# Optimization experiments

Measured on AMD Instinct MI355X. Metric: run time of the kernel, lower is better.

Reference implementation:

```python
import jax, jax.numpy as jnp
import numpy as np

MIN_NORM = 1e-15
BALL_EPS = 1e-5  # keep points strictly inside the unit ball (c = 1)


def _artanh(x):
    return jnp.arctanh(jnp.clip(x, -1.0 + BALL_EPS, 1.0 - BALL_EPS))


def expmap0(u):
    # Poincare ball exp map at the origin, c = 1
    n = jnp.clip(jnp.linalg.norm(u, axis=-1, keepdims=True), MIN_NORM)
    return jnp.tanh(n) * u / n


def mobius_matvec(M, x):
    # Mobius matrix-vector product applied to every row of x: [N, D] -> [N, D]
    x_n = jnp.clip(jnp.linalg.norm(x, axis=-1, keepdims=True), MIN_NORM)
    Mx = x @ M.T
    Mx_n = jnp.clip(jnp.linalg.norm(Mx, axis=-1, keepdims=True), MIN_NORM)
    return jnp.tanh(Mx_n / x_n * _artanh(x_n)) * Mx / Mx_n


def pairwise_sqdist(x):
    # sqdist(x_i, x_j) for all pairs via mobius_add(-x_i, x_j); x: [N, D] -> [N, N]
    u = -x[:, None, :]          # [N, 1, D]
    v = x[None, :, :]           # [1, N, D]
    xy = jnp.sum(u * v, axis=-1, keepdims=True)   # [N, N, 1]
    x2 = jnp.sum(u * u, axis=-1, keepdims=True)
    y2 = jnp.sum(v * v, axis=-1, keepdims=True)
    num = (1.0 + 2.0 * xy + y2) * u + (1.0 - x2) * v   # [N, N, D]
    den = jnp.clip(1.0 + 2.0 * xy + x2 * y2, MIN_NORM)
    ma_n = jnp.linalg.norm(num / den, axis=-1)          # [N, N]
    d = 2.0 * _artanh(ma_n)
    return d * d


def setup_inputs() -> dict:
    key = jax.random.key(0)
    k1, k2, k3 = jax.random.split(key, 3)
    N, D, L = 512, 256, 2
    H_euc = jax.random.normal(k1, (N, D), dtype=jnp.float32)
    att_W = jax.random.normal(k2, (L, D, D), dtype=jnp.float32) / np.sqrt(D)
    A = jax.random.randint(k3, (N, N), 0, 2).astype(bool)
    return {"H_euc": H_euc, "att_W": att_W, "A": A}


def reference(H_euc, att_W, A):
    H = expmap0(H_euc)                      # [N, D] on the Poincare ball
    L = att_W.shape[0]
    for l in range(L):
        Wh = mobius_matvec(att_W[l], H)     # one mobius matvec per node (hoisted out of the i,j loop)
        scores = pairwise_sqdist(Wh)        # [N, N] hyperbolic squared distances
        scores = jnp.where(A, scores, -10000.0)
        att = jax.nn.softmax(scores, axis=1)
        att = jnp.where(A, att, 0.0)
        H = att @ H                         # [N, D]
    return H
```

## Files before the change

kernel.cpp:

```cpp
#include <hip/hip_runtime.h>
#include <math.h>

#define NN 512
#define DD 256

#define FMA4(P, S, V) \
  P.x = fmaf(S, (V).x, P.x); P.y = fmaf(S, (V).y, P.y); \
  P.z = fmaf(S, (V).z, P.z); P.w = fmaf(S, (V).w, P.w);

__device__ __forceinline__ void wred_sum2(double& a, double& b){
  #pragma unroll
  for (int o = 32; o > 0; o >>= 1){
    a += __shfl_down(a, o);
    b += __shfl_down(b, o);
  }
}
__device__ void bred_sum2(double& a, double& b){
  __shared__ double sa[4], sb[4]; __shared__ double ra, rb;
  int lane = threadIdx.x & 63, w = threadIdx.x >> 6;
  wred_sum2(a, b);
  __syncthreads();
  if (lane == 0){ sa[w] = a; sb[w] = b; }
  __syncthreads();
  if (threadIdx.x == 0){
    ra = (sa[0] + sa[1]) + (sa[2] + sa[3]);
    rb = (sb[0] + sb[1]) + (sb[2] + sb[3]);
  }
  __syncthreads();
  a = ra; b = rb;
}

__device__ __forceinline__ double artanh_clip(double x){
  const double lim = 1.0 - 1e-5;
  if (x >  lim) x =  lim;
  if (x < -lim) x = -lim;
  return 0.5 * log((1.0 + x) / (1.0 - x));
}

__global__ __launch_bounds__(256) void transpose_k(const float* __restrict__ W,
                                                   float* __restrict__ W0T,
                                                   float* __restrict__ W1T){
  __shared__ float tile[64][65];
  int b = blockIdx.x, t = threadIdx.x;
  const float* src = (b < 16) ? W : (W + DD * DD);
  float* dst = (b < 16) ? W0T : W1T;
  int tb = b & 15, tr = tb >> 2, tc = tb & 3;
  int tx = t & 63, ty4 = t >> 6;
  #pragma unroll
  for (int yy = 0; yy < 64; yy += 4)
    tile[yy + ty4][tx] = src[(tr * 64 + yy + ty4) * DD + tc * 64 + tx];
  __syncthreads();
  #pragma unroll
  for (int yy = 0; yy < 64; yy += 4)
    dst[(tc * 64 + yy + ty4) * DD + tr * 64 + tx] = tile[tx][yy + ty4];
}

__global__ __launch_bounds__(256) void matvec0_k(
    const float* __restrict__ Hin, const float* __restrict__ W0T,
    float* __restrict__ Hf, float* __restrict__ Wh, float* __restrict__ WhT,
    double* __restrict__ r2){
  int b = blockIdx.x, t = threadIdx.x;
  int i0 = 2 * b, i1 = i0 + 1;
  __shared__ float h0s[DD], h1s[DD];
  __shared__ float4 mp[512];
  float u0 = Hin[i0 * DD + t], u1 = Hin[i1 * DD + t];
  double n0 = (double)u0 * (double)u0, n1 = (double)u1 * (double)u1;
  bred_sum2(n0, n1);
  n0 = sqrt(n0); if (n0 < 1e-15) n0 = 1e-15;
  n1 = sqrt(n1); if (n1 < 1e-15) n1 = 1e-15;
  double t0 = tanh(n0), t1 = tanh(n1);
  float h0 = (float)(t0 / n0 * (double)u0);
  float h1 = (float)(t1 / n1 * (double)u1);
  Hf[i0 * DD + t] = h0; Hf[i1 * DD + t] = h1;
  double xn0 = t0 < 1e-15 ? 1e-15 : t0;
  double xn1 = t1 < 1e-15 ? 1e-15 : t1;
  h0s[t] = h0; h1s[t] = h1;
  __syncthreads();
  {
    int ks = t >> 6, dq = t & 63;
    const float4* WT4 = (const float4*)W0T;
    float4 p0 = {0,0,0,0}, p1 = {0,0,0,0};
    int k0 = ks * 64;
    #pragma unroll 8
    for (int kk = 0; kk < 64; kk++){
      int k = k0 + kk;
      float4 wv = WT4[k * 64 + dq];
      float a0 = h0s[k], a1 = h1s[k];
      FMA4(p0, a0, wv)
      FMA4(p1, a1, wv)
    }
    mp[(ks * 64 + dq) * 2 + 0] = p0;
    mp[(ks * 64 + dq) * 2 + 1] = p1;
  }
  __syncthreads();
  const float* pf = (const float*)mp;
  int base = (t >> 2) * 8 + (t & 3);
  float mx0 = (pf[base]     + pf[base +  512]) + (pf[base + 1024] + pf[base + 1536]);
  float mx1 = (pf[base + 4] + pf[base +  516]) + (pf[base + 1028] + pf[base + 1540]);
  double m0 = (double)mx0 * (double)mx0, m1 = (double)mx1 * (double)mx1;
  bred_sum2(m0, m1);
  double mn0 = sqrt(m0); if (mn0 < 1e-15) mn0 = 1e-15;
  double mn1 = sqrt(m1); if (mn1 < 1e-15) mn1 = 1e-15;
  double th0 = tanh(mn0 / xn0 * artanh_clip(xn0));
  double th1 = tanh(mn1 / xn1 * artanh_clip(xn1));
  float w0 = (float)((double)mx0 * (th0 / mn0));
  float w1 = (float)((double)mx1 * (th1 / mn1));
  Wh[i0 * DD + t] = w0;  Wh[i1 * DD + t] = w1;
  WhT[t * NN + i0] = w0; WhT[t * NN + i1] = w1;
  if (t == 0){ r2[i0] = th0 * th0; r2[i1] = th1 * th1; }
}

template<bool LAST>
__global__ __launch_bounds__(512) void fused_k(
    const float* __restrict__ Wh, const float* __restrict__ WhT,
    const double* __restrict__ r2, const int* __restrict__ A,
    const float* __restrict__ H, const float* __restrict__ WT2,
    float* __restrict__ Hn, float* __restrict__ Whn,
    float* __restrict__ WhTn, double* __restrict__ r2n){
  int b = blockIdx.x, tid = threadIdx.x;
  int i0 = 2 * b;
  __shared__ float xs[2 * DD];
  __shared__ float a_s[2][NN];
  __shared__ float4 parts[1024];
  __shared__ double ssum[8];
  __shared__ float hn_s[2][DD];
  __shared__ double hnorm2[2];

  xs[tid] = Wh[i0 * DD + tid];
  __syncthreads();

  {
    int ks = tid >> 7, jq = tid & 127;
    const float4* WT4 = (const float4*)WhT;
    const float4* x04 = (const float4*)xs;
    const float4* x14 = (const float4*)(xs + DD);
    float4 p0 = {0,0,0,0}, p1 = {0,0,0,0};
    int kq0 = ks * 16;
    #pragma unroll 4
    for (int kk = 0; kk < 16; kk++){
      float4 xa = x04[kq0 + kk], xb = x14[kq0 + kk];
      const float4* wp = WT4 + (kq0 + kk) * 4 * 128 + jq;
      float4 wa = wp[0], wb = wp[128], wc = wp[256], wd = wp[384];
      FMA4(p0, xa.x, wa) FMA4(p0, xa.y, wb) FMA4(p0, xa.z, wc) FMA4(p0, xa.w, wd)
      FMA4(p1, xb.x, wa) FMA4(p1, xb.y, wb) FMA4(p1, xb.z, wc) FMA4(p1, xb.w, wd)
    }
    parts[(ks * 128 + jq) * 2 + 0] = p0;
    parts[(ks * 128 + jq) * 2 + 1] = p1;
  }
  __syncthreads();

  int sgC = tid >> 6, qC = tid & 63;
  const float4* H4 = (const float4*)H;
  float4 hpre[8];
  #pragma unroll
  for (int jj = 0; jj < 8; jj++) hpre[jj] = H4[(sgC * 64 + jj) * 64 + qC];

  int r = tid >> 8, j2 = tid & 255;
  int i = i0 + r;
  double X2 = r2[i];
  const float* pf = (const float*)parts;
  auto dsum = [&](int j) -> double {
    int base = (((j >> 2) * 2 + r) << 2) + (j & 3);
    return ((double)pf[base] + (double)pf[base + 1024])
         + ((double)pf[base + 2048] + (double)pf[base + 3072]);
  };
  double d0 = dsum(j2), d1 = dsum(j2 + 256);

  auto score = [&](double dot, double Y2, int jj) -> double {
    if (i == jj) return 0.0;
    double xy = -dot;
    double a  = 1.0 + 2.0 * xy + Y2;
    double bb = 1.0 - X2;
    double den = 1.0 + 2.0 * xy + X2 * Y2;
    if (den < 1e-15) den = 1e-15;
    double nn = a * a * X2 + 2.0 * a * bb * xy + bb * bb * Y2;
    if (nn < 0.0) nn = 0.0;
    double s = sqrt(nn);
    double smax = den * (1.0 - 1e-5);
    if (s > smax) s = smax;
    double d = log((den + s) / (den - s));
    return d * d;
  };

  double Y0 = r2[j2], Y1 = r2[j2 + 256];
  int m0 = A[i * NN + j2], m1 = A[i * NN + j2 + 256];
  double e0 = 0.0, e1 = 0.0;
  if (m0) e0 = exp(score(d0, Y0, j2) - 150.0);
  if (m1) e1 = exp(score(d1, Y1, j2 + 256) - 150.0);

  double part = e0 + e1;
  #pragma unroll
  for (int o = 32; o > 0; o >>= 1) part += __shfl_down(part, o);
  int w = tid >> 6, lane = tid & 63;
  if (lane == 0) ssum[w] = part;
  __syncthreads();
  int base4 = r * 4;
  double sum = (ssum[base4] + ssum[base4 + 1]) + (ssum[base4 + 2] + ssum[base4 + 3]);
  double inv = 1.0 / sum;
  a_s[r][j2]       = m0 ? (float)(e0 * inv) : 0.f;
  a_s[r][j2 + 256] = m1 ? (float)(e1 * inv) : 0.f;
  __syncthreads();

  {
    float4 c0 = {0,0,0,0}, c1 = {0,0,0,0};
    int jb = sgC * 64;
    #pragma unroll
    for (int jj = 0; jj < 8; jj++){
      int j = jb + jj;
      float a0 = a_s[0][j], a1 = a_s[1][j];
      float4 h = hpre[jj];
      FMA4(c0, a0, h) FMA4(c1, a1, h)
    }
    #pragma unroll 8
    for (int jj = 8; jj < 64; jj++){
      int j = jb + jj;
      float a0 = a_s[0][j], a1 = a_s[1][j];
      float4 h = H4[j * 64 + qC];
      FMA4(c0, a0, h) FMA4(c1, a1, h)
    }
    parts[sgC * 64 + qC]       = c0;
    parts[512 + sgC * 64 + qC] = c1;
  }
  __syncthreads();
  if (tid < 128){
    int rr = tid >> 6, qq = tid & 63;
    float4 p[8];
    #pragma unroll
    for (int s8 = 0; s8 < 8; s8++) p[s8] = parts[rr * 512 + s8 * 64 + qq];
    float4 o;
    o.x = ((p[0].x + p[1].x) + (p[2].x + p[3].x)) + ((p[4].x + p[5].x) + (p[6].x + p[7].x));
    o.y = ((p[0].y + p[1].y) + (p[2].y + p[3].y)) + ((p[4].y + p[5].y) + (p[6].y + p[7].y));
    o.z = ((p[0].z + p[1].z) + (p[2].z + p[3].z)) + ((p[4].z + p[5].z) + (p[6].z + p[7].z));
    o.w = ((p[0].w + p[1].w) + (p[2].w + p[3].w)) + ((p[4].w + p[5].w) + (p[6].w + p[7].w));
    ((float4*)(Hn + (i0 + rr) * DD))[qq] = o;
    if (!LAST){
      ((float4*)hn_s[rr])[qq] = o;
      double s = (double)o.x * o.x + (double)o.y * o.y
               + (double)o.z * o.z + (double)o.w * o.w;
      #pragma unroll
      for (int off = 32; off > 0; off >>= 1) s += __shfl_down(s, off);
      if (qq == 0) hnorm2[rr] = s;
    }
  }
  if (LAST) return;
  __syncthreads();

  {
    int ks2 = tid >> 6, dq = tid & 63;
    const float4* WT4b = (const float4*)WT2;
    const float* h0 = hn_s[0]; const float* h1 = hn_s[1];
    float4 p0 = {0,0,0,0}, p1 = {0,0,0,0};
    int k0 = ks2 * 32;
    #pragma unroll 8
    for (int kk = 0; kk < 32; kk++){
      int k = k0 + kk;
      float4 wv = WT4b[k * 64 + dq];
      float a0v = h0[k], a1v = h1[k];
      FMA4(p0, a0v, wv) FMA4(p1, a1v, wv)
    }
    parts[(ks2 * 64 + dq) * 2 + 0] = p0;
    parts[(ks2 * 64 + dq) * 2 + 1] = p1;
  }
  __syncthreads();
  {
    int rr = tid >> 8, d = tid & 255;
    const float* pf2 = (const float*)parts;
    int base = ((d >> 2) * 2 + rr) * 4 + (d & 3);
    float q0 = pf2[base]        + pf2[base + 512];
    float q1 = pf2[base + 1024] + pf2[base + 1536];
    float q2 = pf2[base + 2048] + pf2[base + 2560];
    float q3 = pf2[base + 3072] + pf2[base + 3584];
    float mx = (q0 + q1) + (q2 + q3);
    double m2 = (double)mx * (double)mx;
    #pragma unroll
    for (int o = 32; o > 0; o >>= 1) m2 += __shfl_down(m2, o);
    int w2 = tid >> 6, lane2 = tid & 63;
    if (lane2 == 0) ssum[w2] = m2;
    __syncthreads();
    int b4 = rr * 4;
    double m2sum = (ssum[b4] + ssum[b4 + 1]) + (ssum[b4 + 2] + ssum[b4 + 3]);
    double mn = sqrt(m2sum); if (mn < 1e-15) mn = 1e-15;
    double xn = sqrt(hnorm2[rr]); if (xn < 1e-15) xn = 1e-15;
    double th = tanh(mn / xn * artanh_clip(xn));
    float wv = (float)((double)mx * (th / mn));
    int irow = i0 + rr;
    Whn[irow * DD + d] = wv;
    WhTn[d * NN + irow] = wv;
    if (d == 0) r2n[irow] = th * th;
  }
}

extern "C" void kernel_launch(void* const* d_in, const int* in_sizes, int n_in,
                              void* d_out, int out_size, void* d_ws, size_t ws_size,
                              hipStream_t stream){
  const float* H_euc = (const float*)d_in[0];
  const float* W     = (const float*)d_in[1];
  const int*   A     = (const int*)d_in[2];
  float* out = (float*)d_out;

  float* Hf   = (float*)d_ws;
  float* Hn   = Hf   + NN * DD;
  float* Wh   = Hn   + NN * DD;
  float* WhT  = Wh   + NN * DD;
  float* Whb  = WhT  + NN * DD;
  float* WhTb = Whb  + NN * DD;
  float* W0T  = WhTb + NN * DD;
  float* W1T  = W0T  + DD * DD;
  double* r2  = (double*)(W1T + DD * DD);
  double* r2b = r2 + NN;

  transpose_k<<<32, 256, 0, stream>>>(W, W0T, W1T);
  matvec0_k<<<NN / 2, 256, 0, stream>>>(H_euc, W0T, Hf, Wh, WhT, r2);
  fused_k<false><<<NN / 2, 2 * DD, 0, stream>>>(Wh, WhT, r2, A, Hf, W1T, Hn, Whb, WhTb, r2b);
  fused_k<true> <<<NN / 2, 2 * DD, 0, stream>>>(Whb, WhTb, r2b, A, Hn, nullptr, out, nullptr, nullptr, nullptr);
}
```

Baseline: 65.15 us.

## Merge all stages into one cooperative kernel with grid-wide syncs

Replaces the four separate launches (transpose, layer-0 matvec, two fused attention layers) with a single cooperative kernel of 256 blocks that uses grid.sync between stages. The layer-0 matvec now reads W rows directly (dot-product per output), which removes the need for a W0 transpose. Wh rows are kept in shared memory across the grid barrier instead of being written to and reread from global memory. This removes launch gaps and some global traffic, at the cost of grid barrier overhead and a different matvec access pattern.

```diff
diff --git a/kernel.cpp b/kernel.cpp
--- a/kernel.cpp
+++ b/kernel.cpp
@@ -1,5 +1,8 @@
 #include <hip/hip_runtime.h>
+#include <hip/hip_cooperative_groups.h>
 #include <math.h>
+
+namespace cg = cooperative_groups;
 
 #define NN 512
 #define DD 256
@@ -8,26 +11,10 @@
   P.x = fmaf(S, (V).x, P.x); P.y = fmaf(S, (V).y, P.y); \
   P.z = fmaf(S, (V).z, P.z); P.w = fmaf(S, (V).w, P.w);
 
-__device__ __forceinline__ void wred_sum2(double& a, double& b){
+__device__ __forceinline__ double wred_sum(double v){
   #pragma unroll
-  for (int o = 32; o > 0; o >>= 1){
-    a += __shfl_down(a, o);
-    b += __shfl_down(b, o);
-  }
-}
-__device__ void bred_sum2(double& a, double& b){
-  __shared__ double sa[4], sb[4]; __shared__ double ra, rb;
-  int lane = threadIdx.x & 63, w = threadIdx.x >> 6;
-  wred_sum2(a, b);
-  __syncthreads();
-  if (lane == 0){ sa[w] = a; sb[w] = b; }
-  __syncthreads();
-  if (threadIdx.x == 0){
-    ra = (sa[0] + sa[1]) + (sa[2] + sa[3]);
-    rb = (sb[0] + sb[1]) + (sb[2] + sb[3]);
-  }
-  __syncthreads();
-  a = ra; b = rb;
+  for (int o = 32; o > 0; o >>= 1) v += __shfl_down(v, o);
+  return v;
 }
 
 __device__ __forceinline__ double artanh_clip(double x){
@@ -37,97 +24,16 @@
   return 0.5 * log((1.0 + x) / (1.0 - x));
 }
 
-__global__ __launch_bounds__(256) void transpose_k(const float* __restrict__ W,
-                                                   float* __restrict__ W0T,
-                                                   float* __restrict__ W1T){
-  __shared__ float tile[64][65];
-  int b = blockIdx.x, t = threadIdx.x;
-  const float* src = (b < 16) ? W : (W + DD * DD);
-  float* dst = (b < 16) ? W0T : W1T;
-  int tb = b & 15, tr = tb >> 2, tc = tb & 3;
-  int tx = t & 63, ty4 = t >> 6;
-  #pragma unroll
-  for (int yy = 0; yy < 64; yy += 4)
-    tile[yy + ty4][tx] = src[(tr * 64 + yy + ty4) * DD + tc * 64 + tx];
-  __syncthreads();
-  #pragma unroll
-  for (int yy = 0; yy < 64; yy += 4)
-    dst[(tc * 64 + yy + ty4) * DD + tr * 64 + tx] = tile[tx][yy + ty4];
-}
-
-__global__ __launch_bounds__(256) void matvec0_k(
-    const float* __restrict__ Hin, const float* __restrict__ W0T,
-    float* __restrict__ Hf, float* __restrict__ Wh, float* __restrict__ WhT,
-    double* __restrict__ r2){
-  int b = blockIdx.x, t = threadIdx.x;
-  int i0 = 2 * b, i1 = i0 + 1;
-  __shared__ float h0s[DD], h1s[DD];
-  __shared__ float4 mp[512];
-  float u0 = Hin[i0 * DD + t], u1 = Hin[i1 * DD + t];
-  double n0 = (double)u0 * (double)u0, n1 = (double)u1 * (double)u1;
-  bred_sum2(n0, n1);
-  n0 = sqrt(n0); if (n0 < 1e-15) n0 = 1e-15;
-  n1 = sqrt(n1); if (n1 < 1e-15) n1 = 1e-15;
-  double t0 = tanh(n0), t1 = tanh(n1);
-  float h0 = (float)(t0 / n0 * (double)u0);
-  float h1 = (float)(t1 / n1 * (double)u1);
-  Hf[i0 * DD + t] = h0; Hf[i1 * DD + t] = h1;
-  double xn0 = t0 < 1e-15 ? 1e-15 : t0;
-  double xn1 = t1 < 1e-15 ? 1e-15 : t1;
-  h0s[t] = h0; h1s[t] = h1;
-  __syncthreads();
-  {
-    int ks = t >> 6, dq = t & 63;
-    const float4* WT4 = (const float4*)W0T;
-    float4 p0 = {0,0,0,0}, p1 = {0,0,0,0};
-    int k0 = ks * 64;
-    #pragma unroll 8
-    for (int kk = 0; kk < 64; kk++){
-      int k = k0 + kk;
-      float4 wv = WT4[k * 64 + dq];
-      float a0 = h0s[k], a1 = h1s[k];
-      FMA4(p0, a0, wv)
-      FMA4(p1, a1, wv)
-    }
-    mp[(ks * 64 + dq) * 2 + 0] = p0;
-    mp[(ks * 64 + dq) * 2 + 1] = p1;
-  }
-  __syncthreads();
-  const float* pf = (const float*)mp;
-  int base = (t >> 2) * 8 + (t & 3);
-  float mx0 = (pf[base]     + pf[base +  512]) + (pf[base + 1024] + pf[base + 1536]);
-  float mx1 = (pf[base + 4] + pf[base +  516]) + (pf[base + 1028] + pf[base + 1540]);
-  double m0 = (double)mx0 * (double)mx0, m1 = (double)mx1 * (double)mx1;
-  bred_sum2(m0, m1);
-  double mn0 = sqrt(m0); if (mn0 < 1e-15) mn0 = 1e-15;
-  double mn1 = sqrt(m1); if (mn1 < 1e-15) mn1 = 1e-15;
-  double th0 = tanh(mn0 / xn0 * artanh_clip(xn0));
-  double th1 = tanh(mn1 / xn1 * artanh_clip(xn1));
-  float w0 = (float)((double)mx0 * (th0 / mn0));
-  float w1 = (float)((double)mx1 * (th1 / mn1));
-  Wh[i0 * DD + t] = w0;  Wh[i1 * DD + t] = w1;
-  WhT[t * NN + i0] = w0; WhT[t * NN + i1] = w1;
-  if (t == 0){ r2[i0] = th0 * th0; r2[i1] = th1 * th1; }
-}
-
 template<bool LAST>
-__global__ __launch_bounds__(512) void fused_k(
-    const float* __restrict__ Wh, const float* __restrict__ WhT,
-    const double* __restrict__ r2, const int* __restrict__ A,
-    const float* __restrict__ H, const float* __restrict__ WT2,
-    float* __restrict__ Hn, float* __restrict__ Whn,
-    float* __restrict__ WhTn, double* __restrict__ r2n){
-  int b = blockIdx.x, tid = threadIdx.x;
+__device__ void fused_body(int b, int tid,
+    const float* __restrict__ WhT, const double* __restrict__ r2,
+    const int* __restrict__ A, const float* __restrict__ H,
+    const float* __restrict__ WT2,
+    float* __restrict__ HnOut, float* __restrict__ WhTn, double* __restrict__ r2n,
+    float* xs, float (*a_s)[NN], float4* parts, double* ssum,
+    float (*hn_s)[DD], double* hnorm2)
+{
   int i0 = 2 * b;
-  __shared__ float xs[2 * DD];
-  __shared__ float a_s[2][NN];
-  __shared__ float4 parts[1024];
-  __shared__ double ssum[8];
-  __shared__ float hn_s[2][DD];
-  __shared__ double hnorm2[2];
-
-  xs[tid] = Wh[i0 * DD + tid];
-  __syncthreads();
 
   {
     int ks = tid >> 7, jq = tid & 127;
@@ -139,7 +45,7 @@
     #pragma unroll 4
     for (int kk = 0; kk < 16; kk++){
       float4 xa = x04[kq0 + kk], xb = x14[kq0 + kk];
-      const float4* wp = WT4 + (kq0 + kk) * 4 * 128 + jq;
+      const float4* wp = WT4 + (kq0 + kk) * 512 + jq;
       float4 wa = wp[0], wb = wp[128], wc = wp[256], wd = wp[384];
       FMA4(p0, xa.x, wa) FMA4(p0, xa.y, wb) FMA4(p0, xa.z, wc) FMA4(p0, xa.w, wd)
       FMA4(p1, xb.x, wa) FMA4(p1, xb.y, wb) FMA4(p1, xb.z, wc) FMA4(p1, xb.w, wd)
@@ -189,8 +95,7 @@
   if (m1) e1 = exp(score(d1, Y1, j2 + 256) - 150.0);
 
   double part = e0 + e1;
-  #pragma unroll
-  for (int o = 32; o > 0; o >>= 1) part += __shfl_down(part, o);
+  part = wred_sum(part);
   int w = tid >> 6, lane = tid & 63;
   if (lane == 0) ssum[w] = part;
   __syncthreads();
@@ -232,7 +137,7 @@
     o.y = ((p[0].y + p[1].y) + (p[2].y + p[3].y)) + ((p[4].y + p[5].y) + (p[6].y + p[7].y));
     o.z = ((p[0].z + p[1].z) + (p[2].z + p[3].z)) + ((p[4].z + p[5].z) + (p[6].z + p[7].z));
     o.w = ((p[0].w + p[1].w) + (p[2].w + p[3].w)) + ((p[4].w + p[5].w) + (p[6].w + p[7].w));
-    ((float4*)(Hn + (i0 + rr) * DD))[qq] = o;
+    ((float4*)(HnOut + (i0 + rr) * DD))[qq] = o;
     if (!LAST){
       ((float4*)hn_s[rr])[qq] = o;
       double s = (double)o.x * o.x + (double)o.y * o.y
@@ -272,8 +177,7 @@
     float q3 = pf2[base + 3072] + pf2[base + 3584];
     float mx = (q0 + q1) + (q2 + q3);
     double m2 = (double)mx * (double)mx;
-    #pragma unroll
-    for (int o = 32; o > 0; o >>= 1) m2 += __shfl_down(m2, o);
+    m2 = wred_sum(m2);
     int w2 = tid >> 6, lane2 = tid & 63;
     if (lane2 == 0) ssum[w2] = m2;
     __syncthreads();
@@ -284,10 +188,94 @@
     double th = tanh(mn / xn * artanh_clip(xn));
     float wv = (float)((double)mx * (th / mn));
     int irow = i0 + rr;
-    Whn[irow * DD + d] = wv;
+    xs[rr * DD + d] = wv;
     WhTn[d * NN + irow] = wv;
     if (d == 0) r2n[irow] = th * th;
   }
+}
+
+__global__ __launch_bounds__(512) void mega_k(
+    const float* __restrict__ Hin, const float* __restrict__ W,
+    const int* __restrict__ A,
+    float* __restrict__ Hf, float* __restrict__ Hn,
+    float* __restrict__ WhT, float* __restrict__ WhTb,
+    float* __restrict__ W1T, double* __restrict__ r2, double* __restrict__ r2b,
+    float* __restrict__ out)
+{
+  cg::grid_group grid = cg::this_grid();
+  int b = blockIdx.x, tid = threadIdx.x;
+  int i0 = 2 * b;
+  __shared__ float xs[2 * DD];
+  __shared__ float a_s[2][NN];
+  __shared__ float4 parts[1024];
+  __shared__ double ssum[8];
+  __shared__ float hn_s[2][DD];
+  __shared__ double hnorm2[2];
+
+  {
+    int r = tid >> 8, t = tid & 255, lane = tid & 63, w = tid >> 6;
+    int irow = i0 + r;
+    float u = Hin[irow * DD + t];
+    double p = (double)u * (double)u;
+    p = wred_sum(p);
+    if (lane == 0) ssum[w] = p;
+    __syncthreads();
+    int b4 = r * 4;
+    double n2 = (ssum[b4] + ssum[b4 + 1]) + (ssum[b4 + 2] + ssum[b4 + 3]);
+    double n = sqrt(n2); if (n < 1e-15) n = 1e-15;
+    double tn = tanh(n);
+    float h = (float)(tn / n * (double)u);
+    Hf[irow * DD + t] = h;
+    xs[r * DD + t] = h;
+    double xn = tn < 1e-15 ? 1e-15 : tn;
+    __syncthreads();
+    const float4* Wt = (const float4*)(W + t * DD);
+    const float4* hr = (const float4*)(xs + r * DD);
+    float4 acc = {0,0,0,0};
+    #pragma unroll 8
+    for (int k = 0; k < DD / 4; k++){
+      float4 wv = Wt[k], x = hr[k];
+      acc.x = fmaf(x.x, wv.x, acc.x); acc.y = fmaf(x.y, wv.y, acc.y);
+      acc.z = fmaf(x.z, wv.z, acc.z); acc.w = fmaf(x.w, wv.w, acc.w);
+    }
+    float mx = (acc.x + acc.y) + (acc.z + acc.w);
+    double m2 = (double)mx * (double)mx;
+    m2 = wred_sum(m2);
+    if (lane == 0) ssum[w] = m2;
+    __syncthreads();
+    double mxn2 = (ssum[b4] + ssum[b4 + 1]) + (ssum[b4 + 2] + ssum[b4 + 3]);
+    double mn = sqrt(mxn2); if (mn < 1e-15) mn = 1e-15;
+    double th = tanh(mn / xn * artanh_clip(xn));
+    float wv = (float)((double)mx * (th / mn));
+    WhT[t * NN + irow] = wv;
+    xs[r * DD + t] = wv;
+    if (t == 0) r2[irow] = th * th;
+  }
+  if (b < 16){
+    float* tf = (float*)parts;
+    const float* W1 = W + DD * DD;
+    int tr = b >> 2, tc = b & 3;
+    int tx = tid & 63, ty = tid >> 6;
+    #pragma unroll
+    for (int yy = 0; yy < 64; yy += 8){
+      int y = yy + ty;
+      tf[y * 64 + (tx ^ y)] = W1[(tr * 64 + y) * DD + tc * 64 + tx];
+    }
+    __syncthreads();
+    #pragma unroll
+    for (int yy = 0; yy < 64; yy += 8){
+      int y = yy + ty;
+      W1T[(tc * 64 + y) * DD + tr * 64 + tx] = tf[tx * 64 + (y ^ tx)];
+    }
+  }
+  grid.sync();
+
+  fused_body<false>(b, tid, WhT, r2, A, Hf, W1T, Hn, WhTb, r2b,
+                    xs, a_s, parts, ssum, hn_s, hnorm2);
+  grid.sync();
+
+  fused_body<true>(b, tid, WhTb, r2b, A, Hn, nullptr, out, nullptr, nullptr,
+                   xs, a_s, parts, ssum, hn_s, hnorm2);
 }
 
 extern "C" void kernel_launch(void* const* d_in, const int* in_sizes, int n_in,
@@ -300,17 +288,17 @@
 
   float* Hf   = (float*)d_ws;
   float* Hn   = Hf   + NN * DD;
-  float* Wh   = Hn   + NN * DD;
-  float* WhT  = Wh   + NN * DD;
-  float* Whb  = WhT  + NN * DD;
-  float* WhTb = Whb  + NN * DD;
-  float* W0T  = WhTb + NN * DD;
-  float* W1T  = W0T  + DD * DD;
+  float* WhT  = Hn   + NN * DD;
+  float* WhTb = WhT  + NN * DD;
+  float* W1T  = WhTb + NN * DD;
   double* r2  = (double*)(W1T + DD * DD);
   double* r2b = r2 + NN;
 
-  transpose_k<<<32, 256, 0, stream>>>(W, W0T, W1T);
-  matvec0_k<<<NN / 2, 256, 0, stream>>>(H_euc, W0T, Hf, Wh, WhT, r2);
-  fused_k<false><<<NN / 2, 2 * DD, 0, stream>>>(Wh, WhT, r2, A, Hf, W1T, Hn, Whb, WhTb, r2b);
-  fused_k<true> <<<NN / 2, 2 * DD, 0, stream>>>(Whb, WhTb, r2b, A, Hn, nullptr, out, nullptr, nullptr, nullptr);
-}
+  void* args[] = {
+    (void*)&H_euc, (void*)&W, (void*)&A,
+    (void*)&Hf, (void*)&Hn, (void*)&WhT, (void*)&WhTb,
+    (void*)&W1T, (void*)&r2, (void*)&r2b, (void*)&out
+  };
+  hipLaunchCooperativeKernel((void*)mega_k, dim3(NN / 2), dim3(512),
+                             args, 0, stream);
+}
```

Result: slower. 138.8 us (+113.1%).
